# Performance work log

Hardware: AMD Instinct MI355X
Metric: run time of the kernel (lower is better)

The kernel has to match this reference:

```python
import jax, jax.numpy as jnp
import numpy as np

B, IN, OUT = 8192, 4096, 4096


def setup_inputs() -> dict:
    key = jax.random.key(0)
    k_x, k_w, k_t, k_n = jax.random.split(key, 4)
    # int8 activations and weights (stored as int8; accumulated in int32)
    x = jax.random.randint(k_x, (B, IN), -128, 128, dtype=jnp.int32).astype(jnp.int8)
    W = jax.random.randint(k_w, (OUT, IN), -128, 128, dtype=jnp.int32).astype(jnp.int8)
    # per-channel BN fold: additive term t (int32) and negative bitshift n
    t = jax.random.randint(k_t, (OUT,), -(1 << 15), 1 << 15, dtype=jnp.int32)
    n = jax.random.randint(k_n, (OUT,), -9, -6, dtype=jnp.int32)  # shift right by 6..8
    act_min = jnp.full((OUT,), -128, dtype=jnp.int32)
    act_max = jnp.full((OUT,), 127, dtype=jnp.int32)
    return {"x": x, "W": W, "t": t, "n": n, "act_min": act_min, "act_max": act_max}


def reference(x, W, t, n, act_min, act_max):
    # int32-accumulate int8 GEMM: F.linear(x, W) -> [B, OUT]
    acc = jnp.matmul(x.astype(jnp.int32), W.astype(jnp.int32).T)
    acc = acc + t  # broadcast per-output-channel bias add
    acc = jnp.right_shift(acc, -n)  # arithmetic right shift requantization
    acc = jnp.clip(acc, act_min, act_max)
    # pure_positive is False (act_min < 0) -> cast to small signed type
    return acc.astype(jnp.int8)
```

## Files before the change

### kernel.cpp

```cpp
#include <hip/hip_runtime.h>
#include <stdint.h>


#define BDIM 8192
#define INDIM 4096
#define OUTDIM 4096

typedef __attribute__((ext_vector_type(4))) int I4;

__global__ __launch_bounds__(256) void pack_frag(const int* __restrict__ x,
                                                 const int* __restrict__ W,
                                                 uint32_t* __restrict__ xp,
                                                 uint32_t* __restrict__ wp) {
    const uint32_t xq = (BDIM / 16) * 64 * 64;
    uint32_t u = blockIdx.x * 256 + threadIdx.x;
    const int* src;
    uint32_t* dst;
    if (u < xq) {
        uint32_t m16 = u >> 12, kb = (u >> 6) & 63, lane = u & 63;
        src = x + (size_t)(m16 * 16 + (lane & 15)) * INDIM + kb * 64 + (lane >> 4) * 16;
        dst = xp + (size_t)u * 4;
    } else {
        uint32_t v = u - xq;
        uint32_t n16 = v >> 12, kb = (v >> 6) & 63, lane = v & 63;
        src = W + (size_t)(n16 * 16 + (lane & 15)) * INDIM + kb * 64 + (lane >> 4) * 16;
        dst = wp + (size_t)v * 4;
    }
    uint32_t ow[4];
#pragma unroll
    for (int q = 0; q < 4; ++q) {
        int4 a = ((const int4*)src)[q];
        ow[q] = ((uint32_t)a.x & 255u)
              | (((uint32_t)a.y & 255u) << 8)
              | (((uint32_t)a.z & 255u) << 16)
              | (((uint32_t)a.w & 255u) << 24);
    }
    *(uint4*)dst = *(uint4*)ow;
}

__global__ __launch_bounds__(256) void gemm_flat(
    const uint8_t* __restrict__ Xp,
    const uint8_t* __restrict__ Wp,
    const int* __restrict__ t, const int* __restrict__ nsh,
    const int* __restrict__ amin, const int* __restrict__ amax,
    int* __restrict__ out) {

    const int bn = blockIdx.x;
    const int bm = blockIdx.y;
    const int tid = threadIdx.x;
    const int w = tid >> 6;
    const int lane = tid & 63;
    const int wm = (w & 1) * 64;
    const int wn = (w >> 1) * 64;
    const int quad = lane >> 4;
    const int rl = lane & 15;

    const uint8_t* pa[4];
    const uint8_t* pb[4];
#pragma unroll
    for (int i = 0; i < 4; ++i)
        pa[i] = Xp + ((size_t)(bm * 8 + (w & 1) * 4 + i) << 16) + lane * 16;
#pragma unroll
    for (int j = 0; j < 4; ++j)
        pb[j] = Wp + ((size_t)(bn * 8 + (w >> 1) * 4 + j) << 16) + lane * 16;

    I4 acc[4][4];
#pragma unroll
    for (int i = 0; i < 4; ++i)
#pragma unroll
        for (int j = 0; j < 4; ++j) acc[i][j] = (I4){0, 0, 0, 0};

    I4 a0[4], b0[4], a1[4], b1[4];
#pragma unroll
    for (int i = 0; i < 4; ++i) a0[i] = *(const I4*)(pa[i]);
#pragma unroll
    for (int j = 0; j < 4; ++j) b0[j] = *(const I4*)(pb[j]);
#pragma unroll
    for (int i = 0; i < 4; ++i) a1[i] = *(const I4*)(pa[i] + 1024);
#pragma unroll
    for (int j = 0; j < 4; ++j) b1[j] = *(const I4*)(pb[j] + 1024);

    for (int kb = 0; kb < 62; kb += 2) {
#pragma unroll
        for (int i = 0; i < 4; ++i)
#pragma unroll
            for (int j = 0; j < 4; ++j)
                acc[i][j] = __builtin_amdgcn_mfma_i32_16x16x64_i8(a0[i], b0[j], acc[i][j], 0, 0, 0);
        const size_t o0 = (size_t)(kb + 2) * 1024;
#pragma unroll
        for (int i = 0; i < 4; ++i) a0[i] = *(const I4*)(pa[i] + o0);
#pragma unroll
        for (int j = 0; j < 4; ++j) b0[j] = *(const I4*)(pb[j] + o0);

#pragma unroll
        for (int i = 0; i < 4; ++i)
#pragma unroll
            for (int j = 0; j < 4; ++j)
                acc[i][j] = __builtin_amdgcn_mfma_i32_16x16x64_i8(a1[i], b1[j], acc[i][j], 0, 0, 0);
        const size_t o1 = (size_t)(kb + 3) * 1024;
#pragma unroll
        for (int i = 0; i < 4; ++i) a1[i] = *(const I4*)(pa[i] + o1);
#pragma unroll
        for (int j = 0; j < 4; ++j) b1[j] = *(const I4*)(pb[j] + o1);

        __builtin_amdgcn_s_barrier();
    }
#pragma unroll
    for (int i = 0; i < 4; ++i)
#pragma unroll
        for (int j = 0; j < 4; ++j)
            acc[i][j] = __builtin_amdgcn_mfma_i32_16x16x64_i8(a0[i], b0[j], acc[i][j], 0, 0, 0);
#pragma unroll
    for (int i = 0; i < 4; ++i)
#pragma unroll
        for (int j = 0; j < 4; ++j)
            acc[i][j] = __builtin_amdgcn_mfma_i32_16x16x64_i8(a1[i], b1[j], acc[i][j], 0, 0, 0);

#pragma unroll
    for (int j = 0; j < 4; ++j) {
        const int o = bn * 128 + wn + j * 16 + rl;
        const int tt = t[o];
        const int sh = -nsh[o];
        const int mn = amin[o];
        const int mx = amax[o];
#pragma unroll
        for (int i = 0; i < 4; ++i) {
            const int rowbase = bm * 128 + wm + i * 16 + quad * 4;
#pragma unroll
            for (int r = 0; r < 4; ++r) {
                int v = acc[i][j][r] + tt;
                v >>= sh;
                v = v < mn ? mn : (v > mx ? mx : v);
                __builtin_nontemporal_store(v, &out[(size_t)(rowbase + r) * OUTDIM + o]);
            }
        }
    }
}

extern "C" void kernel_launch(void* const* d_in, const int* in_sizes, int n_in,
                              void* d_out, int out_size, void* d_ws, size_t ws_size,
                              hipStream_t stream) {
    const int* x = (const int*)d_in[0];
    const int* W = (const int*)d_in[1];
    const int* t = (const int*)d_in[2];
    const int* n = (const int*)d_in[3];
    const int* amin = (const int*)d_in[4];
    const int* amax = (const int*)d_in[5];
    int* out = (int*)d_out;

    uint8_t* xp = (uint8_t*)d_ws;
    uint8_t* wp = xp + (size_t)BDIM * INDIM;

    {
        int nthreads = (BDIM / 16) * 64 * 64 + (OUTDIM / 16) * 64 * 64;
        pack_frag<<<nthreads / 256, 256, 0, stream>>>(x, W, (uint32_t*)xp, (uint32_t*)wp);
    }

    dim3 grid(OUTDIM / 128, BDIM / 128);
    gemm_flat<<<grid, 256, 0, stream>>>(xp, wp, t, n, amin, amax, out);
}
```

Before: 417.6 us.

## Switch GEMM to 32x32x32 int8 MFMA with 256x128 block tiles

Repacks the int8 operands into 32-row fragments matching the 32x32x32 MFMA layout and rewrites the GEMM to use that instruction. Block tiles grow from 128x128 to 256x128, with the grid reordered so M varies fastest and occupancy hinted at 2 blocks per CU. This aims to cut the number of MFMA issues and raise operand reuse per global load. The cost is 64 accumulator VGPRs per wave, which may pressure registers, and an epilogue store pattern that scatters across more rows.

```diff
diff --git a/kernel.cpp b/kernel.cpp
--- a/kernel.cpp
+++ b/kernel.cpp
@@ -7,23 +7,24 @@
 #define OUTDIM 4096
 
 typedef __attribute__((ext_vector_type(4))) int I4;
+typedef __attribute__((ext_vector_type(16))) int I16;
 
-__global__ __launch_bounds__(256) void pack_frag(const int* __restrict__ x,
-                                                 const int* __restrict__ W,
-                                                 uint32_t* __restrict__ xp,
-                                                 uint32_t* __restrict__ wp) {
-    const uint32_t xq = (BDIM / 16) * 64 * 64;
+__global__ __launch_bounds__(256) void pack_frag32(const int* __restrict__ x,
+                                                   const int* __restrict__ W,
+                                                   uint32_t* __restrict__ xp,
+                                                   uint32_t* __restrict__ wp) {
+    const uint32_t xq = (BDIM / 32) * 128 * 64;
     uint32_t u = blockIdx.x * 256 + threadIdx.x;
     const int* src;
     uint32_t* dst;
     if (u < xq) {
-        uint32_t m16 = u >> 12, kb = (u >> 6) & 63, lane = u & 63;
-        src = x + (size_t)(m16 * 16 + (lane & 15)) * INDIM + kb * 64 + (lane >> 4) * 16;
+        uint32_t m32 = u >> 13, kb = (u >> 6) & 127, lane = u & 63;
+        src = x + (size_t)(m32 * 32 + (lane & 31)) * INDIM + kb * 32 + (lane >> 5) * 16;
         dst = xp + (size_t)u * 4;
     } else {
         uint32_t v = u - xq;
-        uint32_t n16 = v >> 12, kb = (v >> 6) & 63, lane = v & 63;
-        src = W + (size_t)(n16 * 16 + (lane & 15)) * INDIM + kb * 64 + (lane >> 4) * 16;
+        uint32_t n32 = v >> 13, kb = (v >> 6) & 127, lane = v & 63;
+        src = W + (size_t)(n32 * 32 + (lane & 31)) * INDIM + kb * 32 + (lane >> 5) * 16;
         dst = wp + (size_t)v * 4;
     }
     uint32_t ow[4];
@@ -38,100 +39,101 @@
     *(uint4*)dst = *(uint4*)ow;
 }
 
-__global__ __launch_bounds__(256) void gemm_flat(
+__global__ __launch_bounds__(256, 2) void gemm_flat32(
     const uint8_t* __restrict__ Xp,
     const uint8_t* __restrict__ Wp,
     const int* __restrict__ t, const int* __restrict__ nsh,
     const int* __restrict__ amin, const int* __restrict__ amax,
     int* __restrict__ out) {
 
-    const int bn = blockIdx.x;
-    const int bm = blockIdx.y;
+    const int bm = blockIdx.x;
+    const int bn = blockIdx.y;
     const int tid = threadIdx.x;
     const int w = tid >> 6;
     const int lane = tid & 63;
-    const int wm = (w & 1) * 64;
-    const int wn = (w >> 1) * 64;
-    const int quad = lane >> 4;
-    const int rl = lane & 15;
+    const int wr = w >> 1;
+    const int wc = w & 1;
 
     const uint8_t* pa[4];
-    const uint8_t* pb[4];
+    const uint8_t* pb[2];
 #pragma unroll
     for (int i = 0; i < 4; ++i)
-        pa[i] = Xp + ((size_t)(bm * 8 + (w & 1) * 4 + i) << 16) + lane * 16;
+        pa[i] = Xp + ((size_t)(bm * 8 + wr * 4 + i) << 17) + lane * 16;
 #pragma unroll
-    for (int j = 0; j < 4; ++j)
-        pb[j] = Wp + ((size_t)(bn * 8 + (w >> 1) * 4 + j) << 16) + lane * 16;
+    for (int j = 0; j < 2; ++j)
+        pb[j] = Wp + ((size_t)(bn * 4 + wc * 2 + j) << 17) + lane * 16;
 
-    I4 acc[4][4];
+    I16 acc[4][2];
 #pragma unroll
     for (int i = 0; i < 4; ++i)
 #pragma unroll
-        for (int j = 0; j < 4; ++j) acc[i][j] = (I4){0, 0, 0, 0};
+        for (int j = 0; j < 2; ++j)
+#pragma unroll
+            for (int r = 0; r < 16; ++r) acc[i][j][r] = 0;
 
-    I4 a0[4], b0[4], a1[4], b1[4];
+    I4 a0[4], b0[2], a1[4], b1[2];
 #pragma unroll
     for (int i = 0; i < 4; ++i) a0[i] = *(const I4*)(pa[i]);
 #pragma unroll
-    for (int j = 0; j < 4; ++j) b0[j] = *(const I4*)(pb[j]);
+    for (int j = 0; j < 2; ++j) b0[j] = *(const I4*)(pb[j]);
 #pragma unroll
     for (int i = 0; i < 4; ++i) a1[i] = *(const I4*)(pa[i] + 1024);
 #pragma unroll
-    for (int j = 0; j < 4; ++j) b1[j] = *(const I4*)(pb[j] + 1024);
+    for (int j = 0; j < 2; ++j) b1[j] = *(const I4*)(pb[j] + 1024);
 
-    for (int kb = 0; kb < 62; kb += 2) {
+    for (int kb = 0; kb < 126; kb += 2) {
 #pragma unroll
         for (int i = 0; i < 4; ++i)
 #pragma unroll
-            for (int j = 0; j < 4; ++j)
-                acc[i][j] = __builtin_amdgcn_mfma_i32_16x16x64_i8(a0[i], b0[j], acc[i][j], 0, 0, 0);
+            for (int j = 0; j < 2; ++j)
+                acc[i][j] = __builtin_amdgcn_mfma_i32_32x32x32_i8(a0[i], b0[j], acc[i][j], 0, 0, 0);
         const size_t o0 = (size_t)(kb + 2) * 1024;
 #pragma unroll
         for (int i = 0; i < 4; ++i) a0[i] = *(const I4*)(pa[i] + o0);
 #pragma unroll
-        for (int j = 0; j < 4; ++j) b0[j] = *(const I4*)(pb[j] + o0);
+        for (int j = 0; j < 2; ++j) b0[j] = *(const I4*)(pb[j] + o0);
 
 #pragma unroll
         for (int i = 0; i < 4; ++i)
 #pragma unroll
-            for (int j = 0; j < 4; ++j)
-                acc[i][j] = __builtin_amdgcn_mfma_i32_16x16x64_i8(a1[i], b1[j], acc[i][j], 0, 0, 0);
+            for (int j = 0; j < 2; ++j)
+                acc[i][j] = __builtin_amdgcn_mfma_i32_32x32x32_i8(a1[i], b1[j], acc[i][j], 0, 0, 0);
         const size_t o1 = (size_t)(kb + 3) * 1024;
 #pragma unroll
         for (int i = 0; i < 4; ++i) a1[i] = *(const I4*)(pa[i] + o1);
 #pragma unroll
-        for (int j = 0; j < 4; ++j) b1[j] = *(const I4*)(pb[j] + o1);
+        for (int j = 0; j < 2; ++j) b1[j] = *(const I4*)(pb[j] + o1);
 
         __builtin_amdgcn_s_barrier();
     }
 #pragma unroll
     for (int i = 0; i < 4; ++i)
 #pragma unroll
-        for (int j = 0; j < 4; ++j)
-            acc[i][j] = __builtin_amdgcn_mfma_i32_16x16x64_i8(a0[i], b0[j], acc[i][j], 0, 0, 0);
+        for (int j = 0; j < 2; ++j)
+            acc[i][j] = __builtin_amdgcn_mfma_i32_32x32x32_i8(a0[i], b0[j], acc[i][j], 0, 0, 0);
 #pragma unroll
     for (int i = 0; i < 4; ++i)
 #pragma unroll
-        for (int j = 0; j < 4; ++j)
-            acc[i][j] = __builtin_amdgcn_mfma_i32_16x16x64_i8(a1[i], b1[j], acc[i][j], 0, 0, 0);
+        for (int j = 0; j < 2; ++j)
+            acc[i][j] = __builtin_amdgcn_mfma_i32_32x32x32_i8(a1[i], b1[j], acc[i][j], 0, 0, 0);
 
 #pragma unroll
-    for (int j = 0; j < 4; ++j) {
-        const int o = bn * 128 + wn + j * 16 + rl;
+    for (int j = 0; j < 2; ++j) {
+        const int o = bn * 128 + wc * 64 + j * 32 + (lane & 31);
         const int tt = t[o];
         const int sh = -nsh[o];
         const int mn = amin[o];
         const int mx = amax[o];
 #pragma unroll
         for (int i = 0; i < 4; ++i) {
-            const int rowbase = bm * 128 + wm + i * 16 + quad * 4;
+            const int rowbase = bm * 256 + wr * 128 + i * 32 + 4 * (lane >> 5);
 #pragma unroll
-            for (int r = 0; r < 4; ++r) {
+            for (int r = 0; r < 16; ++r) {
+                const int row = rowbase + (r & 3) + 8 * (r >> 2);
                 int v = acc[i][j][r] + tt;
                 v >>= sh;
                 v = v < mn ? mn : (v > mx ? mx : v);
-                __builtin_nontemporal_store(v, &out[(size_t)(rowbase + r) * OUTDIM + o]);
+                __builtin_nontemporal_store(v, &out[(size_t)row * OUTDIM + o]);
             }
         }
     }
@@ -152,10 +154,10 @@
     uint8_t* wp = xp + (size_t)BDIM * INDIM;
 
     {
-        int nthreads = (BDIM / 16) * 64 * 64 + (OUTDIM / 16) * 64 * 64;
-        pack_frag<<<nthreads / 256, 256, 0, stream>>>(x, W, (uint32_t*)xp, (uint32_t*)wp);
+        int nthreads = (BDIM / 32) * 128 * 64 + (OUTDIM / 32) * 128 * 64;
+        pack_frag32<<<nthreads / 256, 256, 0, stream>>>(x, W, (uint32_t*)xp, (uint32_t*)wp);
     }
 
-    dim3 grid(OUTDIM / 128, BDIM / 128);
-    gemm_flat<<<grid, 256, 0, stream>>>(xp, wp, t, n, amin, amax, out);
+    dim3 grid(BDIM / 256, OUTDIM / 128);
+    gemm_flat32<<<grid, 256, 0, stream>>>(xp, wp, t, n, amin, amax, out);
 }
```

Measured after the change: 407.8 us. -2.4%, faster.
